# Kernel tuning notes

Hardware: AMD Instinct MI355X
Metric: run time of the kernel (lower is better)

Reference implementation:

```python
import jax, jax.numpy as jnp
import numpy as np

N = 16384
MUL0, MUL1, MUL2 = 128, 64, 32            # multiplicities of 0e, 1e, 2e
A = 16                                    # node_attr_dim (Ax0e)
D0, D1, D2 = MUL0, MUL1 * 3, MUL2 * 5     # e3nn flat block sizes
DIN = D0 + D1 + D2                        # 480
NGATE = MUL1 + MUL2                       # 96 gate scalars
OUT0 = MUL0 + NGATE                       # 224 scalar (0e) outputs of fctp_1


def setup_inputs() -> dict:
    key = jax.random.key(0)
    ks = jax.random.split(key, 10)
    f32 = jnp.float32
    return {
        "node_vec": jax.random.normal(ks[0], (N, DIN), f32),
        "node_embedding": jax.random.normal(ks[1], (N, A), f32),
        # fctp_1 path weights (fully-connected TP with Ax0e attr)
        "W1_l0": jax.random.normal(ks[2], (MUL0, A, OUT0), f32),
        "W1_l1": jax.random.normal(ks[3], (MUL1, A, MUL1), f32),
        "W1_l2": jax.random.normal(ks[4], (MUL2, A, MUL2), f32),
        "b1": jnp.zeros((OUT0,), f32),
        # fctp_2 scalar-path weight (only 0e x 0e -> 0e path exists)
        "W2": jax.random.normal(ks[5], (MUL0, A, A), f32),
        "b2": jnp.zeros((A,), f32),
        # scalar readout MLP: LinearRS -> SiLU -> LinearRS
        "W3": jax.random.normal(ks[6], (A, A), f32),
        "b3": jnp.zeros((A,), f32),
        "W4": jax.random.normal(ks[7], (A, 1), f32),
        "b4": jnp.zeros((1,), f32),
    }


def reference(node_vec, node_embedding, W1_l0, W1_l1, W1_l2, b1, W2, b2, W3, b3, W4, b4):
    # split e3nn-layout features into per-l blocks [N, mul, 2l+1]
    x0 = node_vec[:, :D0]                               # [N, 128]   l=0
    x1 = node_vec[:, D0:D0 + D1].reshape(-1, MUL1, 3)   # [N, 64, 3] l=1
    x2 = node_vec[:, D0 + D1:].reshape(-1, MUL2, 5)     # [N, 32, 5] l=2
    a = node_embedding                                  # [N, A] 0e scalars
    # fctp_1: fully-connected TP with Ax0e attr -> per-l bilinear mix (path-normalized)
    s = jnp.einsum('ni,na,iak->nk', x0, a, W1_l0) / np.sqrt(MUL0 * A) + b1  # [N, 224]
    y1 = jnp.einsum('nim,na,iak->nkm', x1, a, W1_l1) / np.sqrt(MUL1 * A)    # [N, 64, 3]
    y2 = jnp.einsum('nim,na,iak->nkm', x2, a, W1_l2) / np.sqrt(MUL2 * A)    # [N, 32, 5]
    # SwishGate: SiLU on scalars, sigmoid gates multiply the l>0 channels
    scalars = jax.nn.silu(s[:, :MUL0])
    gates = jax.nn.sigmoid(s[:, MUL0:])
    y1 = y1 * gates[:, :MUL1, None]
    y2 = y2 * gates[:, MUL1:, None]
    # fctp_2: output irreps = Ax0e, so only the 0e x 0e -> 0e path exists;
    # the gated l>0 features have no path to 0e (same as the torch TP).
    mid = jnp.einsum('ni,na,iak->nk', scalars, a, W2) / np.sqrt(MUL0 * A) + b2  # [N, A]
    # output_network: LinearRS -> SiLU -> LinearRS (rescale 1/sqrt(fan_in))
    h = jax.nn.silu(mid @ W3 / np.sqrt(A) + b3)
    return h @ W4 / np.sqrt(A) + b4                     # [N, 1]
```

## Files before the change

kernel.cpp:

```cpp
#include <hip/hip_runtime.h>


#define NKC 64

typedef _Float16 h8 __attribute__((ext_vector_type(8)));
typedef _Float16 h4 __attribute__((ext_vector_type(4)));
typedef _Float16 h2 __attribute__((ext_vector_type(2)));
typedef float    f32x4 __attribute__((ext_vector_type(4)));

static __device__ __forceinline__ unsigned int pack2h(float a, float b) {
    h2 t = {(_Float16)a, (_Float16)b};
    return __builtin_bit_cast(unsigned int, t);
}
static __device__ __forceinline__ f32x4 mfma_h(uint4 a, uint4 b, f32x4 c) {
    return __builtin_amdgcn_mfma_f32_16x16x32_f16(
        __builtin_bit_cast(h8, a), __builtin_bit_cast(h8, b), c, 0, 0, 0);
}
static __device__ __forceinline__ uint4 mk_afrag(_Float16 xh, const h2* ee) {
    h2 xx = {xh, xh};
    uint4 r;
    r.x = __builtin_bit_cast(unsigned int, (h2)(xx * ee[0]));
    r.y = __builtin_bit_cast(unsigned int, (h2)(xx * ee[1]));
    r.z = __builtin_bit_cast(unsigned int, (h2)(xx * ee[2]));
    r.w = __builtin_bit_cast(unsigned int, (h2)(xx * ee[3]));
    return r;
}

__global__ __launch_bounds__(256) void prep_kernel(
        const float* __restrict__ W1, const float* __restrict__ W2,
        _Float16* __restrict__ W1T, _Float16* __restrict__ W2T) {
    const int b = blockIdx.x, kc = b >> 2, tp = b & 3;
    const int tid = threadIdx.x;
    __shared__ float l1[32 * 36];
    __shared__ float l2[32 * 20];

    {
        int row = tid >> 3, c4 = tid & 7;
        float4 v = *(const float4*)(W1 + (size_t)(kc * 32 + row) * 224 + tp * 32 + c4 * 4);
        *(float4*)(l1 + row * 36 + c4 * 4) = v;
    }
    if (tp == 0 && tid < 128) {
        int row = tid >> 2, c4 = tid & 3;
        float4 v = *(const float4*)(W2 + (size_t)(kc * 32 + row) * 16 + c4 * 4);
        *(float4*)(l2 + row * 20 + c4 * 4) = v;
    }
    __syncthreads();

    if (tid < 128) {
        int tl = tid >> 6, t = tp * 2 + tl, lane = tid & 63;
        int q = lane >> 4, cc = lane & 15, colL = tl * 16 + cc;
        unsigned int w[4];
#pragma unroll
        for (int jj = 0; jj < 4; ++jj)
            w[jj] = pack2h(l1[(q * 8 + 2 * jj) * 36 + colL],
                           l1[(q * 8 + 2 * jj + 1) * 36 + colL]);
        *(uint4*)(W1T + (size_t)kc * 4096 + (t * 64 + lane) * 8) =
            make_uint4(w[0], w[1], w[2], w[3]);
    }
    if (tp == 0 && tid >= 128 && tid < 192) {
        int lane = tid - 128, q = lane >> 4, cc = lane & 15;
        unsigned int w[4];
#pragma unroll
        for (int jj = 0; jj < 4; ++jj)
            w[jj] = pack2h(l2[(q * 8 + 2 * jj) * 20 + cc],
                           l2[(q * 8 + 2 * jj + 1) * 20 + cc]);
        *(uint4*)(W2T + (size_t)kc * 512 + lane * 8) = make_uint4(w[0], w[1], w[2], w[3]);
    }
}

__global__ __launch_bounds__(512, 4) void main_kernel(
        const float* __restrict__ node_vec, const float* __restrict__ emb,
        const _Float16* __restrict__ W1T, const _Float16* __restrict__ W2T,
        const float* __restrict__ b1, const float* __restrict__ b2,
        const float* __restrict__ W3, const float* __restrict__ b3,
        const float* __restrict__ W4, const float* __restrict__ b4,
        float* __restrict__ out) {
    const int tid  = threadIdx.x;
    const int wave = tid >> 6, lane = tid & 63;
    const int q = lane >> 4, c = lane & 15;
    const int ih = q >> 1;
    const int aodd = q & 1;
    const int mh = wave >> 2;
    const int cq = wave & 3;
    const int nodeBase = blockIdx.x * 32;

    __shared__ _Float16 x0e[32 * 72];
    __shared__ _Float16 x0o[32 * 72];
    __shared__ _Float16 sce[32 * 72];
    __shared__ _Float16 sco[32 * 72];
    __shared__ float    midp[4 * 32 * 17];
    __shared__ float    mids[32 * 17];
    __shared__ float    w3s[256];
    __shared__ float    b3s[16];
    __shared__ float    w4s[16];
    __shared__ float    b4s[1];

    for (int idx = tid; idx < 1024; idx += 512) {
        int row = idx >> 5, c4 = idx & 31;
        float4 v = *(const float4*)(node_vec + (size_t)(nodeBase + row) * 480 + c4 * 4);
        h2 ev = {(_Float16)v.x, (_Float16)v.z};
        h2 ov = {(_Float16)v.y, (_Float16)v.w};
        *(h2*)(x0e + row * 72 + c4 * 2) = ev;
        *(h2*)(x0o + row * 72 + c4 * 2) = ov;
    }
    if (tid < 256) w3s[tid] = W3[tid];
    if (tid < 16) { b3s[tid] = b3[tid]; w4s[tid] = W4[tid]; }
    if (tid == 0) b4s[0] = b4[0];

    h2 ee[4];
    {
        const float* ep = emb + (size_t)(nodeBase + mh * 16 + c) * 16 + aodd * 8;
        float4 v0 = *(const float4*)ep;
        float4 v1 = *(const float4*)(ep + 4);
        ee[0] = (h2){(_Float16)v0.x, (_Float16)v0.y};
        ee[1] = (h2){(_Float16)v0.z, (_Float16)v0.w};
        ee[2] = (h2){(_Float16)v1.x, (_Float16)v1.y};
        ee[3] = (h2){(_Float16)v1.z, (_Float16)v1.w};
    }
    __syncthreads();

    f32x4 acc0 = (f32x4){0.f, 0.f, 0.f, 0.f};
    f32x4 acc1 = (f32x4){0.f, 0.f, 0.f, 0.f};

    const uint4* bp = (const uint4*)W1T + cq * 128 + lane;
    const _Float16* xrow = (ih ? x0o : x0e) + (mh * 16 + c) * 72;

    uint4 B0[8], B1[8];
    h4 xa, xb;

#define LOADG(B, X, g)                                                         \
    {                                                                          \
        _Pragma("unroll")                                                      \
        for (int u = 0; u < 4; ++u) {                                          \
            B[2 * u]     = bp[(4 * (g) + u) * 512];                            \
            B[2 * u + 1] = bp[(4 * (g) + u) * 512 + 64];                       \
        }                                                                      \
        X = *(const h4*)(xrow + 4 * (g));                                      \
    }
#define DOG(B, X)                                                              \
    {                                                                          \
        _Pragma("unroll")                                                      \
        for (int u = 0; u < 4; ++u) {                                          \
            uint4 af = mk_afrag(X[u], ee);                                     \
            acc0 = mfma_h(af, B[2 * u], acc0);                                 \
            acc1 = mfma_h(af, B[2 * u + 1], acc1);                             \
        }                                                                      \
    }

    LOADG(B0, xa, 0);
    for (int it = 0; it < 8; ++it) {
        LOADG(B1, xb, 2 * it + 1);
        DOG(B0, xa);
        int g2 = (2 * it + 2) & 15;
        LOADG(B0, xa, g2);
        DOG(B1, xb);
    }
#undef LOADG
#undef DOG

    const float inv2048 = 0.022097086912079608f;
#pragma unroll
    for (int tt = 0; tt < 2; ++tt) {
        int t = cq * 2 + tt;
        float bb1v = b1[t * 16 + c];
        const f32x4& av = tt ? acc1 : acc0;
        _Float16* dst = (c & 1) ? sco : sce;
        int colh = t * 8 + (c >> 1);
#pragma unroll
        for (int r = 0; r < 4; ++r) {
            int node = mh * 16 + q * 4 + r;
            float s  = av[r] * inv2048 + bb1v;
            float sc = s / (1.f + __expf(-s));
            dst[node * 72 + colh] = (_Float16)sc;
        }
    }
    __syncthreads();

    {
        const int ks = cq;
        const _Float16* srow = (ih ? sco : sce) + (mh * 16 + c) * 72 + ks * 16;
        h8 sx0 = *(const h8*)(srow);
        h8 sx1 = *(const h8*)(srow + 8);
        const uint4* b2p = (const uint4*)W2T + lane;
        f32x4 macc = (f32x4){0.f, 0.f, 0.f, 0.f};
        uint4 wb[4];
#pragma unroll
        for (int u = 0; u < 4; ++u) wb[u] = b2p[(ks * 16 + u) * 64];
#pragma unroll
        for (int k2 = 0; k2 < 16; ++k2) {
            uint4 cur = wb[k2 & 3];
            if (k2 + 4 < 16) wb[k2 & 3] = b2p[(ks * 16 + k2 + 4) * 64];
            _Float16 sv = (k2 < 8) ? sx0[k2] : sx1[k2 - 8];
            macc = mfma_h(mk_afrag(sv, ee), cur, macc);
        }
#pragma unroll
        for (int r = 0; r < 4; ++r) {
            int node = mh * 16 + q * 4 + r;
            midp[(ks * 32 + node) * 17 + c] = macc[r];
        }
    }
    __syncthreads();

    {
        int node = tid >> 4, col = tid & 15;
        float m = midp[node * 17 + col] + midp[(32 + node) * 17 + col]
                + midp[(64 + node) * 17 + col] + midp[(96 + node) * 17 + col];
        mids[node * 17 + col] = m * inv2048 + b2[col];
    }
    __syncthreads();

    {
        int n = tid >> 4, jj = tid & 15;
        float a = 0.f;
#pragma unroll
        for (int cc = 0; cc < 16; ++cc) a += mids[n * 17 + cc] * w3s[cc * 16 + jj];
        a = a * 0.25f + b3s[jj];
        float hh = a / (1.f + __expf(-a));
        float po = hh * w4s[jj];
        po += __shfl_xor(po, 1);
        po += __shfl_xor(po, 2);
        po += __shfl_xor(po, 4);
        po += __shfl_xor(po, 8);
        if (jj == 0) out[nodeBase + n] = po * 0.25f + b4s[0];
    }
}

extern "C" void kernel_launch(void* const* d_in, const int* in_sizes, int n_in,
                              void* d_out, int out_size, void* d_ws, size_t ws_size,
                              hipStream_t stream) {
    const float* node_vec = (const float*)d_in[0];
    const float* emb      = (const float*)d_in[1];
    const float* W1       = (const float*)d_in[2];
    const float* b1v      = (const float*)d_in[5];
    const float* W2       = (const float*)d_in[6];
    const float* b2v      = (const float*)d_in[7];
    const float* W3       = (const float*)d_in[8];
    const float* b3v      = (const float*)d_in[9];
    const float* W4       = (const float*)d_in[10];
    const float* b4v      = (const float*)d_in[11];

    _Float16* W1T = (_Float16*)d_ws;
    _Float16* W2T = W1T + 64 * 4096;
    float* out = (float*)d_out;

    prep_kernel<<<256, 256, 0, stream>>>(W1, W2, W1T, W2T);
    main_kernel<<<512, 512, 0, stream>>>(node_vec, emb, W1T, W2T,
                                         b1v, b2v, W3, b3v, W4, b4v, out);
}
```

Baseline: 116.7 us.

## Stage W1 tiles in LDS via async global-to-LDS loads with 64-node blocks

The main kernel now processes 64 nodes per 1024-thread block. The fp16 W1 fragments are streamed into a double-buffered LDS region with global_load_lds, so each weight chunk is fetched once per block and shared by all waves, instead of every wave reading it from global memory into registers. Shared memory is aliased: the x buffers are reused for the gated scalars and the weight buffer for the partial mid sums. The cost is a __syncthreads in each of the 32 chunk iterations, larger blocks that may reduce occupancy, and the latency of the async copies on the critical path.

```diff
diff --git a/kernel.cpp b/kernel.cpp
--- a/kernel.cpp
+++ b/kernel.cpp
@@ -4,13 +4,13 @@
 #define NKC 64
 
 typedef _Float16 h8 __attribute__((ext_vector_type(8)));
-typedef _Float16 h4 __attribute__((ext_vector_type(4)));
 typedef _Float16 h2 __attribute__((ext_vector_type(2)));
 typedef float    f32x4 __attribute__((ext_vector_type(4)));
-
-static __device__ __forceinline__ unsigned int pack2h(float a, float b) {
+typedef unsigned int u32;
+
+static __device__ __forceinline__ u32 pack2h(float a, float b) {
     h2 t = {(_Float16)a, (_Float16)b};
-    return __builtin_bit_cast(unsigned int, t);
+    return __builtin_bit_cast(u32, t);
 }
 static __device__ __forceinline__ f32x4 mfma_h(uint4 a, uint4 b, f32x4 c) {
     return __builtin_amdgcn_mfma_f32_16x16x32_f16(
@@ -19,11 +19,16 @@
 static __device__ __forceinline__ uint4 mk_afrag(_Float16 xh, const h2* ee) {
     h2 xx = {xh, xh};
     uint4 r;
-    r.x = __builtin_bit_cast(unsigned int, (h2)(xx * ee[0]));
-    r.y = __builtin_bit_cast(unsigned int, (h2)(xx * ee[1]));
-    r.z = __builtin_bit_cast(unsigned int, (h2)(xx * ee[2]));
-    r.w = __builtin_bit_cast(unsigned int, (h2)(xx * ee[3]));
+    r.x = __builtin_bit_cast(u32, (h2)(xx * ee[0]));
+    r.y = __builtin_bit_cast(u32, (h2)(xx * ee[1]));
+    r.z = __builtin_bit_cast(u32, (h2)(xx * ee[2]));
+    r.w = __builtin_bit_cast(u32, (h2)(xx * ee[3]));
     return r;
+}
+static __device__ __forceinline__ void async16(const void* g, void* l) {
+    __builtin_amdgcn_global_load_lds(
+        (const __attribute__((address_space(1))) u32*)g,
+        (__attribute__((address_space(3))) u32*)l, 16, 0, 0);
 }
 
 __global__ __launch_bounds__(256) void prep_kernel(
@@ -49,7 +54,7 @@
     if (tid < 128) {
         int tl = tid >> 6, t = tp * 2 + tl, lane = tid & 63;
         int q = lane >> 4, cc = lane & 15, colL = tl * 16 + cc;
-        unsigned int w[4];
+        u32 w[4];
 #pragma unroll
         for (int jj = 0; jj < 4; ++jj)
             w[jj] = pack2h(l1[(q * 8 + 2 * jj) * 36 + colL],
@@ -59,7 +64,7 @@
     }
     if (tp == 0 && tid >= 128 && tid < 192) {
         int lane = tid - 128, q = lane >> 4, cc = lane & 15;
-        unsigned int w[4];
+        u32 w[4];
 #pragma unroll
         for (int jj = 0; jj < 4; ++jj)
             w[jj] = pack2h(l2[(q * 8 + 2 * jj) * 20 + cc],
@@ -68,40 +73,40 @@
     }
 }
 
-__global__ __launch_bounds__(512, 4) void main_kernel(
+__global__ __launch_bounds__(1024, 4) void main_kernel(
         const float* __restrict__ node_vec, const float* __restrict__ emb,
         const _Float16* __restrict__ W1T, const _Float16* __restrict__ W2T,
         const float* __restrict__ b1, const float* __restrict__ b2,
         const float* __restrict__ W3, const float* __restrict__ b3,
         const float* __restrict__ W4, const float* __restrict__ b4,
         float* __restrict__ out) {
+    __shared__ __align__(16) char smem[52368];
+    char*     ldsB = smem;
+    _Float16* xe   = (_Float16*)(smem + 32768);
+    _Float16* xo   = (_Float16*)(smem + 41984);
+    float*    midp = (float*)smem;
+    float*    mids = (float*)(smem + 17408);
+    float*    w3s  = (float*)(smem + 51200);
+    float*    b3s  = (float*)(smem + 52224);
+    float*    w4s  = (float*)(smem + 52288);
+    float*    b4s  = (float*)(smem + 52352);
+
     const int tid  = threadIdx.x;
     const int wave = tid >> 6, lane = tid & 63;
     const int q = lane >> 4, c = lane & 15;
     const int ih = q >> 1;
     const int aodd = q & 1;
-    const int mh = wave >> 2;
+    const int g  = wave >> 2;
     const int cq = wave & 3;
-    const int nodeBase = blockIdx.x * 32;
-
-    __shared__ _Float16 x0e[32 * 72];
-    __shared__ _Float16 x0o[32 * 72];
-    __shared__ _Float16 sce[32 * 72];
-    __shared__ _Float16 sco[32 * 72];
-    __shared__ float    midp[4 * 32 * 17];
-    __shared__ float    mids[32 * 17];
-    __shared__ float    w3s[256];
-    __shared__ float    b3s[16];
-    __shared__ float    w4s[16];
-    __shared__ float    b4s[1];
-
-    for (int idx = tid; idx < 1024; idx += 512) {
+    const int nodeBase = blockIdx.x * 64;
+
+    for (int idx = tid; idx < 2048; idx += 1024) {
         int row = idx >> 5, c4 = idx & 31;
         float4 v = *(const float4*)(node_vec + (size_t)(nodeBase + row) * 480 + c4 * 4);
         h2 ev = {(_Float16)v.x, (_Float16)v.z};
         h2 ov = {(_Float16)v.y, (_Float16)v.w};
-        *(h2*)(x0e + row * 72 + c4 * 2) = ev;
-        *(h2*)(x0o + row * 72 + c4 * 2) = ov;
+        *(h2*)(xe + row * 72 + c4 * 2) = ev;
+        *(h2*)(xo + row * 72 + c4 * 2) = ov;
     }
     if (tid < 256) w3s[tid] = W3[tid];
     if (tid < 16) { b3s[tid] = b3[tid]; w4s[tid] = W4[tid]; }
@@ -109,7 +114,7 @@
 
     h2 ee[4];
     {
-        const float* ep = emb + (size_t)(nodeBase + mh * 16 + c) * 16 + aodd * 8;
+        const float* ep = emb + (size_t)(nodeBase + g * 16 + c) * 16 + aodd * 8;
         float4 v0 = *(const float4*)ep;
         float4 v1 = *(const float4*)(ep + 4);
         ee[0] = (h2){(_Float16)v0.x, (_Float16)v0.y};
@@ -117,46 +122,36 @@
         ee[2] = (h2){(_Float16)v1.x, (_Float16)v1.y};
         ee[3] = (h2){(_Float16)v1.z, (_Float16)v1.w};
     }
-    __syncthreads();
 
     f32x4 acc0 = (f32x4){0.f, 0.f, 0.f, 0.f};
     f32x4 acc1 = (f32x4){0.f, 0.f, 0.f, 0.f};
 
-    const uint4* bp = (const uint4*)W1T + cq * 128 + lane;
-    const _Float16* xrow = (ih ? x0o : x0e) + (mh * 16 + c) * 72;
-
-    uint4 B0[8], B1[8];
-    h4 xa, xb;
-
-#define LOADG(B, X, g)                                                         \
-    {                                                                          \
-        _Pragma("unroll")                                                      \
-        for (int u = 0; u < 4; ++u) {                                          \
-            B[2 * u]     = bp[(4 * (g) + u) * 512];                            \
-            B[2 * u + 1] = bp[(4 * (g) + u) * 512 + 64];                       \
-        }                                                                      \
-        X = *(const h4*)(xrow + 4 * (g));                                      \
-    }
-#define DOG(B, X)                                                              \
-    {                                                                          \
-        _Pragma("unroll")                                                      \
-        for (int u = 0; u < 4; ++u) {                                          \
-            uint4 af = mk_afrag(X[u], ee);                                     \
-            acc0 = mfma_h(af, B[2 * u], acc0);                                 \
-            acc1 = mfma_h(af, B[2 * u + 1], acc1);                             \
-        }                                                                      \
-    }
-
-    LOADG(B0, xa, 0);
-    for (int it = 0; it < 8; ++it) {
-        LOADG(B1, xb, 2 * it + 1);
-        DOG(B0, xa);
-        int g2 = (2 * it + 2) & 15;
-        LOADG(B0, xa, g2);
-        DOG(B1, xb);
-    }
-#undef LOADG
-#undef DOG
+    const int klw = wave >> 3, tw = wave & 7;
+    const char* srcBase = (const char*)W1T + (size_t)((klw * 8 + tw) * 1024) + lane * 16;
+    char* dstBase = ldsB + wave * 1024;
+
+    const _Float16* xrow = (ih ? xo : xe) + (g * 16 + c) * 72;
+    const int fo0 = (cq * 2) * 1024 + lane * 16;
+    const int fo1 = (cq * 2 + 1) * 1024 + lane * 16;
+
+    async16(srcBase, dstBase);
+    __syncthreads();
+
+    for (int ch = 0; ch < 32; ++ch) {
+        if (ch + 1 < 32)
+            async16(srcBase + (size_t)(ch + 1) * 16384, dstBase + ((ch + 1) & 1) * 16384);
+        const char* buf = ldsB + (ch & 1) * 16384;
+        h2 xx = *(const h2*)(xrow + 2 * ch);
+#pragma unroll
+        for (int kl = 0; kl < 2; ++kl) {
+            uint4 f0 = *(const uint4*)(buf + kl * 8192 + fo0);
+            uint4 f1 = *(const uint4*)(buf + kl * 8192 + fo1);
+            uint4 af = mk_afrag(xx[kl], ee);
+            acc0 = mfma_h(af, f0, acc0);
+            acc1 = mfma_h(af, f1, acc1);
+        }
+        __syncthreads();
+    }
 
     const float inv2048 = 0.022097086912079608f;
 #pragma unroll
@@ -164,11 +159,11 @@
         int t = cq * 2 + tt;
         float bb1v = b1[t * 16 + c];
         const f32x4& av = tt ? acc1 : acc0;
-        _Float16* dst = (c & 1) ? sco : sce;
+        _Float16* dst = (c & 1) ? xo : xe;
         int colh = t * 8 + (c >> 1);
 #pragma unroll
         for (int r = 0; r < 4; ++r) {
-            int node = mh * 16 + q * 4 + r;
+            int node = g * 16 + q * 4 + r;
             float s  = av[r] * inv2048 + bb1v;
             float sc = s / (1.f + __expf(-s));
             dst[node * 72 + colh] = (_Float16)sc;
@@ -178,7 +173,7 @@
 
     {
         const int ks = cq;
-        const _Float16* srow = (ih ? sco : sce) + (mh * 16 + c) * 72 + ks * 16;
+        const _Float16* srow = (ih ? xo : xe) + (g * 16 + c) * 72 + ks * 16;
         h8 sx0 = *(const h8*)(srow);
         h8 sx1 = *(const h8*)(srow + 8);
         const uint4* b2p = (const uint4*)W2T + lane;
@@ -195,16 +190,16 @@
         }
 #pragma unroll
         for (int r = 0; r < 4; ++r) {
-            int node = mh * 16 + q * 4 + r;
-            midp[(ks * 32 + node) * 17 + c] = macc[r];
+            int node = g * 16 + q * 4 + r;
+            midp[(ks * 64 + node) * 17 + c] = macc[r];
         }
     }
     __syncthreads();
 
     {
         int node = tid >> 4, col = tid & 15;
-        float m = midp[node * 17 + col] + midp[(32 + node) * 17 + col]
-                + midp[(64 + node) * 17 + col] + midp[(96 + node) * 17 + col];
+        float m = midp[node * 17 + col] + midp[(64 + node) * 17 + col]
+                + midp[(128 + node) * 17 + col] + midp[(192 + node) * 17 + col];
         mids[node * 17 + col] = m * inv2048 + b2[col];
     }
     __syncthreads();
@@ -244,6 +239,6 @@
     float* out = (float*)d_out;
 
     prep_kernel<<<256, 256, 0, stream>>>(W1, W2, W1T, W2T);
-    main_kernel<<<512, 512, 0, stream>>>(node_vec, emb, W1T, W2T,
-                                         b1v, b2v, W3, b3v, W4, b4v, out);
-}
+    main_kernel<<<256, 1024, 0, stream>>>(node_vec, emb, W1T, W2T,
+                                          b1v, b2v, W3, b3v, W4, b4v, out);
+}
```

New measurement: 115.2 us. No clear change (-1.2%).
